# Optimization experiments

Measured on AMD Instinct MI355X. Metric: run time of the kernel, lower is better.

The kernel has to match this reference:

```python
import jax, jax.numpy as jnp
import numpy as np

B, N, E = 8, 10000, 320000
IN_DIM, E_H, E_OUT, OUT_DIM = 16, 32, 32, 32
D_EDGE_IN = IN_DIM * 2 + 2 + 1  # src feats + tgt feats + edge_attr_norm(2) + edge_weight(1)


def setup_inputs() -> dict:
    key = jax.random.key(0)
    ks = jax.random.split(key, 10)
    x = jax.random.normal(ks[0], (B, N, IN_DIM), dtype=jnp.float32)
    edge_index = jax.random.randint(ks[1], (2, E), 0, N)
    # col 0 = city_dist (kept >= 0.5 to avoid divide-by-tiny), col 1 = city_direc
    edge_attr = jax.random.uniform(ks[2], (E, 2), dtype=jnp.float32) + 0.5
    wind_mean = jax.random.normal(ks[3], (2,), dtype=jnp.float32)
    wind_std = jax.random.uniform(ks[4], (2,), dtype=jnp.float32) + 0.5
    def lin(k, fo, fi):
        return jax.random.normal(k, (fo, fi), dtype=jnp.float32) / np.sqrt(fi).astype(np.float32)
    W1 = lin(ks[5], E_H, D_EDGE_IN); b1 = jnp.zeros((E_H,), jnp.float32)
    W2 = lin(ks[6], E_OUT, E_H);     b2 = jnp.zeros((E_OUT,), jnp.float32)
    W3 = lin(ks[7], OUT_DIM, E_OUT); b3 = jnp.zeros((OUT_DIM,), jnp.float32)
    return dict(x=x, edge_attr=edge_attr, wind_mean=wind_mean, wind_std=wind_std,
                W1=W1, b1=b1, W2=W2, b2=b2, W3=W3, b3=b3, edge_index=edge_index)


def reference(x, edge_attr, wind_mean, wind_std, W1, b1, W2, b2, W3, b3, edge_index):
    edge_src, edge_tgt = edge_index[0], edge_index[1]
    node_src = x[:, edge_src]   # [B, E, D] gather
    node_tgt = x[:, edge_tgt]   # [B, E, D]
    # de-normalize wind (last two feature channels of source node)
    src_wind = node_src[:, :, -2:] * wind_std[None, None, :] + wind_mean[None, None, :]
    src_wind_speed = src_wind[:, :, 0]
    src_wind_direc = src_wind[:, :, 1]
    city_dist = edge_attr[:, 0][None, :]   # [1, E]
    city_direc = edge_attr[:, 1][None, :]
    theta = jnp.abs(city_direc - src_wind_direc)                       # [B, E]
    edge_weight = jax.nn.relu(3.0 * src_wind_speed * jnp.cos(theta * 360.0 / 16.0) / city_dist)
    # normalization of edge_attr uses torch's unbiased std (ddof=1)
    ea_norm = (edge_attr - edge_attr.mean(axis=0)) / edge_attr.std(axis=0, ddof=1)  # [E, 2]
    feat = jnp.concatenate([
        node_src, node_tgt,
        jnp.broadcast_to(ea_norm[None], (node_src.shape[0], E, 2)),
        edge_weight[:, :, None],
    ], axis=-1)                                                        # [B, E, D_EDGE_IN]
    h = jax.nn.sigmoid(jnp.einsum('bef,hf->beh', feat, W1) + b1)       # edge MLP
    h = jax.nn.sigmoid(jnp.einsum('beh,oh->beo', h, W2) + b2)          # [B, E, E_OUT]
    agg = jnp.zeros((x.shape[0], x.shape[1], h.shape[-1]), h.dtype).at[:, edge_tgt].add(h)
    out = jax.nn.sigmoid(jnp.einsum('bno,po->bnp', agg, W3) + b3)      # node MLP -> [B, N, OUT_DIM]
    return out
```

## Files before the change

kernel.cpp:

```cpp
#include <hip/hip_runtime.h>
#include <hip/hip_fp16.h>
#include <cmath>

constexpr int Bc = 8;
constexpr int Nn = 10000;
constexpr int Ec = 320000;
constexpr int IN = 16;
constexpr int EH = 32;
constexpr int EO = 32;
constexpr int OD = 32;

constexpr size_t U_CNT = 8;
constexpr size_t U_CUR = U_CNT + Nn;
constexpr size_t U_REC = 20016;
constexpr size_t U_PA  = U_REC + 4 * (size_t)Ec;
constexpr size_t U_PB  = U_PA + (size_t)Bc * Nn * 16;
constexpr size_t U_PW  = U_PB + (size_t)Bc * Nn * 16;

typedef short bf16x8 __attribute__((ext_vector_type(8)));
typedef float f32x4 __attribute__((ext_vector_type(4)));

__device__ __forceinline__ float sigmoid_f(float x) {
    return __builtin_amdgcn_rcpf(1.0f + __expf(-x));
}
__device__ __forceinline__ unsigned bf16r(float f) {
    unsigned u = __builtin_bit_cast(unsigned, f);
    return (u + 0x7FFFu + ((u >> 16) & 1u)) >> 16;
}
__device__ __forceinline__ unsigned bf16pk(float lo, float hi) {
    return bf16r(lo) | (bf16r(hi) << 16);
}

__global__ __launch_bounds__(256) void stats_hist_kernel(const float* __restrict__ ea,
                                                         const int* __restrict__ ei,
                                                         float* __restrict__ ws) {
    int* cnt = (int*)ws + U_CNT;
    float s0 = 0.f, s1 = 0.f, q0 = 0.f, q1 = 0.f;
    for (int i = blockIdx.x * blockDim.x + threadIdx.x; i < Ec; i += gridDim.x * blockDim.x) {
        float2 v = reinterpret_cast<const float2*>(ea)[i];
        s0 += v.x; s1 += v.y; q0 += v.x * v.x; q1 += v.y * v.y;
        atomicAdd(&cnt[ei[Ec + i]], 1);
    }
#pragma unroll
    for (int off = 32; off > 0; off >>= 1) {
        s0 += __shfl_down(s0, off);
        s1 += __shfl_down(s1, off);
        q0 += __shfl_down(q0, off);
        q1 += __shfl_down(q1, off);
    }
    if ((threadIdx.x & 63) == 0) {
        atomicAdd(&ws[0], s0);
        atomicAdd(&ws[1], s1);
        atomicAdd(&ws[2], q0);
        atomicAdd(&ws[3], q1);
    }
}

__global__ void scan_kernel(float* __restrict__ ws) {
    const int tid = threadIdx.x;
    const int lane = tid & 63;
    const int w = tid >> 6;
    if (tid == 0) {
        float s0 = ws[0], s1 = ws[1], q0 = ws[2], q1 = ws[3];
        float m0 = s0 / (float)Ec, m1 = s1 / (float)Ec;
        float v0 = (q0 - s0 * m0) / (float)(Ec - 1);
        float v1 = (q1 - s1 * m1) / (float)(Ec - 1);
        ws[4] = m0; ws[5] = m1;
        ws[6] = rsqrtf(v0); ws[7] = rsqrtf(v1);
    }
    int* cnt    = (int*)ws + U_CNT;
    int* cursor = (int*)ws + U_CUR;
    __shared__ int wtot[4];
    constexpr int CHUNK = 2560;
    const int lo = w * CHUNK;
    const int hi = min(Nn, lo + CHUNK);
    int sum = 0;
    for (int i = lo + lane; i < hi; i += 64) sum += cnt[i];
#pragma unroll
    for (int off = 32; off > 0; off >>= 1) sum += __shfl_down(sum, off);
    if (lane == 0) wtot[w] = sum;
    __syncthreads();
    int carry = 0;
    for (int k = 0; k < w; ++k) carry += wtot[k];
    for (int base = lo; base < hi; base += 64) {
        const int idx = base + lane;
        const int c = (idx < hi) ? cnt[idx] : 0;
        int v = c;
#pragma unroll
        for (int off = 1; off < 64; off <<= 1) {
            int u = __shfl_up(v, off);
            if (lane >= off) v += u;
        }
        if (idx < hi) cursor[idx] = carry + v - c;
        carry += __shfl(v, 63);
    }
}

__global__ __launch_bounds__(256) void record_kernel(const int* __restrict__ ei,
                                                     const float* __restrict__ ea,
                                                     float* __restrict__ ws) {
    int* cursor = (int*)ws + U_CUR;
    uint4* rec  = reinterpret_cast<uint4*>((unsigned*)ws + U_REC);
    const int e = blockIdx.x * 256 + threadIdx.x;
    const int src = ei[e];
    const int tgt = ei[Ec + e];
    const float2 v = reinterpret_cast<const float2*>(ea)[e];
    const int pos = atomicAdd(&cursor[tgt], 1);
    rec[pos] = make_uint4((unsigned)src, (unsigned)tgt,
                          __builtin_bit_cast(unsigned, v.x),
                          __builtin_bit_cast(unsigned, v.y));
}

__global__ __launch_bounds__(256) void precompute_kernel(
    const float* __restrict__ x, const float* __restrict__ wmean,
    const float* __restrict__ wstd, const float* __restrict__ W1,
    const float* __restrict__ b1, float* __restrict__ ws)
{
    const int idx = blockIdx.x * 256 + threadIdx.x;
    if (idx >= Bc * Nn) return;
    const float4* xr = reinterpret_cast<const float4*>(x + (size_t)idx * IN);
    float xv[16];
    float4 t;
    t = xr[0]; xv[0]  = t.x; xv[1]  = t.y; xv[2]  = t.z; xv[3]  = t.w;
    t = xr[1]; xv[4]  = t.x; xv[5]  = t.y; xv[6]  = t.z; xv[7]  = t.w;
    t = xr[2]; xv[8]  = t.x; xv[9]  = t.y; xv[10] = t.z; xv[11] = t.w;
    t = xr[3]; xv[12] = t.x; xv[13] = t.y; xv[14] = t.z; xv[15] = t.w;

    __half2* PA = reinterpret_cast<__half2*>((unsigned*)ws + U_PA) + (size_t)idx * 16;
    __half2* PB = reinterpret_cast<__half2*>((unsigned*)ws + U_PB) + (size_t)idx * 16;
#pragma unroll
    for (int p = 0; p < 16; ++p) {
        float a[2], bb[2];
#pragma unroll
        for (int j = 0; j < 2; ++j) {
            const int o = 2 * p + j;
            const float* wr = W1 + o * 35;
            float av = 0.f, bv = b1[o];
#pragma unroll
            for (int f = 0; f < 16; ++f) {
                av += xv[f] * wr[f];
                bv += xv[f] * wr[16 + f];
            }
            a[j] = av; bb[j] = bv;
        }
        PA[p] = __half2{__float2half(a[0]), __float2half(a[1])};
        PB[p] = __half2{__float2half(bb[0]), __float2half(bb[1])};
    }
    float2* PW = reinterpret_cast<float2*>((unsigned*)ws + U_PW);
    PW[idx] = make_float2(3.0f * (xv[14] * wstd[0] + wmean[0]),
                          xv[15] * wstd[1] + wmean[1]);
}

__global__ __launch_bounds__(256, 4) void edge_kernel(
    const float* __restrict__ W1, const float* __restrict__ W2,
    const float* __restrict__ b2, const float* __restrict__ ws,
    float* __restrict__ agg)
{
    __shared__ unsigned lds[4 * 2560];
    const int tid  = threadIdx.x;
    const int lane = tid & 63;
    const int wid  = tid >> 6;
    unsigned* wl = lds + wid * 2560;

    const int bid = blockIdx.x;
    const int b   = bid & 7;
    const int gid = (bid >> 3) * 256 + wid * 64 + lane;

    const unsigned* wsu = (const unsigned*)ws;
    const uint4 rec = reinterpret_cast<const uint4*>(wsu + U_REC)[gid];
    const int src = (int)rec.x;
    const int tgt = (int)rec.y;
    const float eax = __builtin_bit_cast(float, rec.z);
    const float eay = __builtin_bit_cast(float, rec.w);

    const float2 pw = reinterpret_cast<const float2*>(wsu + U_PW)[b * Nn + src];
    const float theta = fabsf(eay - pw.y);
    const float ewt = fmaxf(pw.x * __cosf(theta * 22.5f) * __builtin_amdgcn_rcpf(eax), 0.0f);
    const float f32v = (eax - ws[4]) * ws[6];
    const float f33v = (eay - ws[5]) * ws[7];

    const uint4* pa4 = reinterpret_cast<const uint4*>(wsu + U_PA + ((size_t)b * Nn + src) * 16);
    const uint4* pb4 = reinterpret_cast<const uint4*>(wsu + U_PB + ((size_t)b * Nn + tgt) * 16);

    unsigned hw[16];
#pragma unroll
    for (int q = 0; q < 4; ++q) {
        const uint4 ua = pa4[q];
        const uint4 ub = pb4[q];
        const unsigned au[4] = {ua.x, ua.y, ua.z, ua.w};
        const unsigned bu[4] = {ub.x, ub.y, ub.z, ub.w};
#pragma unroll
        for (int j = 0; j < 4; ++j) {
            const int p = 4 * q + j;
            const __half2 s = __hadd2(__builtin_bit_cast(__half2, au[j]),
                                      __builtin_bit_cast(__half2, bu[j]));
            const float2 f = __half22float2(s);
            const int o0 = 2 * p, o1 = 2 * p + 1;
            const float acc0 = f.x + f32v * W1[o0 * 35 + 32]
                                   + f33v * W1[o0 * 35 + 33]
                                   + ewt  * W1[o0 * 35 + 34];
            const float acc1 = f.y + f32v * W1[o1 * 35 + 32]
                                   + f33v * W1[o1 * 35 + 33]
                                   + ewt  * W1[o1 * 35 + 34];
            hw[p] = bf16pk(sigmoid_f(acc0), sigmoid_f(acc1));
        }
    }
    {
        uint4* hrow = reinterpret_cast<uint4*>(wl + lane * 20);
#pragma unroll
        for (int q = 0; q < 4; ++q)
            hrow[q] = make_uint4(hw[4*q], hw[4*q+1], hw[4*q+2], hw[4*q+3]);
    }

    const int tprev = __shfl_up(tgt, 1);
    const bool head = (lane == 0) || (tprev != tgt);
    const unsigned long long mask = __ballot(head);
    const unsigned long long mle = (~0ULL) >> (63 - lane);
    const int run = __popcll(mask & mle) - 1;
    const int nruns = __popcll(mask);
    wl[2432 + lane] = (unsigned)run;
    if (head) wl[2496 + run] = (unsigned)tgt;

    const int c16 = lane & 15;
    const int hq  = lane >> 4;

    bf16x8 bw[2];
#pragma unroll
    for (int t = 0; t < 2; ++t) {
        const float* wr = W2 + (c16 + 16 * t) * 32 + 8 * hq;
        const float4 w0 = *reinterpret_cast<const float4*>(wr);
        const float4 w1 = *reinterpret_cast<const float4*>(wr + 4);
        const uint4 pk = make_uint4(bf16pk(w0.x, w0.y), bf16pk(w0.z, w0.w),
                                    bf16pk(w1.x, w1.y), bf16pk(w1.z, w1.w));
        bw[t] = __builtin_bit_cast(bf16x8, pk);
    }

    f32x4 c[4][2];
#pragma unroll
    for (int m = 0; m < 4; ++m) {
        const uint4 av = *reinterpret_cast<const uint4*>(wl + (16 * m + c16) * 20 + 4 * hq);
        const bf16x8 afr = __builtin_bit_cast(bf16x8, av);
#pragma unroll
        for (int t = 0; t < 2; ++t) {
            f32x4 z = {0.f, 0.f, 0.f, 0.f};
            c[m][t] = __builtin_amdgcn_mfma_f32_16x16x32_bf16(afr, bw[t], z, 0, 0, 0);
        }
    }

    const float b2v[2] = { b2[c16], b2[c16 + 16] };
#pragma unroll
    for (int m = 0; m < 4; ++m) {
#pragma unroll
        for (int t = 0; t < 2; ++t) {
            const float v0 = sigmoid_f(c[m][t][0] + b2v[t]);
            const float v1 = sigmoid_f(c[m][t][1] + b2v[t]);
            const float v2 = sigmoid_f(c[m][t][2] + b2v[t]);
            const float v3 = sigmoid_f(c[m][t][3] + b2v[t]);
            const uint2 pk = make_uint2(bf16pk(v0, v1), bf16pk(v2, v3));
            *reinterpret_cast<uint2*>(wl + 1280 + (c16 + 16 * t) * 36 + 8 * m + 2 * hq) = pk;
        }
    }

    bf16x8 vb[2][2];
    unsigned rid[2][8];
#pragma unroll
    for (int kk = 0; kk < 2; ++kk) {
#pragma unroll
        for (int t = 0; t < 2; ++t) {
            const uint4 vv = *reinterpret_cast<const uint4*>(wl + 1280 + (c16 + 16 * t) * 36 + 16 * kk + 4 * hq);
            vb[kk][t] = __builtin_bit_cast(bf16x8, vv);
        }
        const uint4 r0 = *reinterpret_cast<const uint4*>(wl + 2432 + 32 * kk + 8 * hq);
        const uint4 r1 = *reinterpret_cast<const uint4*>(wl + 2432 + 32 * kk + 8 * hq + 4);
        rid[kk][0] = r0.x; rid[kk][1] = r0.y; rid[kk][2] = r0.z; rid[kk][3] = r0.w;
        rid[kk][4] = r1.x; rid[kk][5] = r1.y; rid[kk][6] = r1.z; rid[kk][7] = r1.w;
    }

    const int nm = (nruns + 15) >> 4;
    for (int mr = 0; mr < nm; ++mr) {
        const unsigned rowg = (unsigned)(16 * mr + c16);
        f32x4 d0 = {0.f, 0.f, 0.f, 0.f};
        f32x4 d1 = {0.f, 0.f, 0.f, 0.f};
#pragma unroll
        for (int kk = 0; kk < 2; ++kk) {
            unsigned iw[4];
#pragma unroll
            for (int w = 0; w < 4; ++w) {
                iw[w] = (rid[kk][2 * w]     == rowg ? 0x3f80u : 0u)
                      | (rid[kk][2 * w + 1] == rowg ? 0x3f800000u : 0u);
            }
            const bf16x8 ifr = __builtin_bit_cast(bf16x8, make_uint4(iw[0], iw[1], iw[2], iw[3]));
            d0 = __builtin_amdgcn_mfma_f32_16x16x32_bf16(ifr, vb[kk][0], d0, 0, 0, 0);
            d1 = __builtin_amdgcn_mfma_f32_16x16x32_bf16(ifr, vb[kk][1], d1, 0, 0, 0);
        }
#pragma unroll
        for (int r = 0; r < 4; ++r) {
            const int rn = 16 * mr + 4 * hq + r;
            const unsigned tr = wl[2496 + (rn & 63)];
            if (rn < nruns) {
                float* dst = agg + ((size_t)b * Nn + tr) * 32;
                atomicAdd(dst + c16,      d0[r]);
                atomicAdd(dst + c16 + 16, d1[r]);
            }
        }
    }
}

__global__ __launch_bounds__(256) void node_kernel(
    const float* __restrict__ W3, const float* __restrict__ b3,
    float* __restrict__ out)
{
    const int idx = blockIdx.x * 256 + threadIdx.x;
    if (idx >= Bc * Nn) return;
    float* row = out + (size_t)idx * OD;

    float a[EO];
#pragma unroll
    for (int i = 0; i < EO / 4; ++i) {
        float4 t = reinterpret_cast<float4*>(row)[i];
        a[4 * i] = t.x; a[4 * i + 1] = t.y; a[4 * i + 2] = t.z; a[4 * i + 3] = t.w;
    }
    float r[OD];
#pragma unroll
    for (int p = 0; p < OD; ++p) {
        const float* wr = W3 + p * EO;
        float s = b3[p];
#pragma unroll
        for (int o = 0; o < EO; ++o) s += a[o] * wr[o];
        r[p] = sigmoid_f(s);
    }
#pragma unroll
    for (int i = 0; i < OD / 4; ++i) {
        float4 t;
        t.x = r[4 * i + 0]; t.y = r[4 * i + 1];
        t.z = r[4 * i + 2]; t.w = r[4 * i + 3];
        reinterpret_cast<float4*>(row)[i] = t;
    }
}

extern "C" void kernel_launch(void* const* d_in, const int* in_sizes, int n_in,
                              void* d_out, int out_size, void* d_ws, size_t ws_size,
                              hipStream_t stream) {
    const float* x     = (const float*)d_in[0];
    const float* ea    = (const float*)d_in[1];
    const float* wmean = (const float*)d_in[2];
    const float* wstd  = (const float*)d_in[3];
    const float* W1    = (const float*)d_in[4];
    const float* b1    = (const float*)d_in[5];
    const float* W2    = (const float*)d_in[6];
    const float* b2    = (const float*)d_in[7];
    const float* W3    = (const float*)d_in[8];
    const float* b3    = (const float*)d_in[9];
    const int*   ei    = (const int*)d_in[10];
    float* out = (float*)d_out;
    float* ws  = (float*)d_ws;

    hipMemsetAsync(d_out, 0, (size_t)out_size * sizeof(float), stream);
    hipMemsetAsync(d_ws, 0, (U_CNT + Nn) * sizeof(float), stream);

    stats_hist_kernel<<<256, 256, 0, stream>>>(ea, ei, ws);
    scan_kernel<<<1, 256, 0, stream>>>(ws);
    record_kernel<<<Ec / 256, 256, 0, stream>>>(ei, ea, ws);
    precompute_kernel<<<(Bc * Nn + 255) / 256, 256, 0, stream>>>(x, wmean, wstd, W1, b1, ws);
    edge_kernel<<<(Ec / 256) * Bc, 256, 0, stream>>>(W1, W2, b2, ws, out);
    node_kernel<<<(Bc * Nn + 255) / 256, 256, 0, stream>>>(W3, b3, out);
}
```

Before: 234.0 us.

## Merge histogram, node precompute and output zeroing into one prep kernel; widen scan

Folds the edge-attribute stats/histogram, per-node W1 precompute and the output memset into a single launch whose blocks are partitioned by role. This cuts two launches and a memset and lets the independent stages run concurrently on the GPU. The single-block prefix scan moves from 256 threads looping over 64-wide chunks to 1024 threads, each doing a 10-element serial scan followed by wave and block scans, which shortens the serial scan latency. Mixing heterogeneous block roles in one grid can create some load imbalance.

```diff
diff --git a/kernel.cpp b/kernel.cpp
--- a/kernel.cpp
+++ b/kernel.cpp
@@ -17,6 +17,10 @@
 constexpr size_t U_PB  = U_PA + (size_t)Bc * Nn * 16;
 constexpr size_t U_PW  = U_PB + (size_t)Bc * Nn * 16;
 
+constexpr int HIST_BLOCKS = 256;
+constexpr int PRE_BLOCKS  = (Bc * Nn + 255) / 256;
+constexpr int ZERO_BLOCKS = 512;
+
 typedef short bf16x8 __attribute__((ext_vector_type(8)));
 typedef float f32x4 __attribute__((ext_vector_type(4)));
 
@@ -31,32 +35,84 @@
     return bf16r(lo) | (bf16r(hi) << 16);
 }
 
-__global__ __launch_bounds__(256) void stats_hist_kernel(const float* __restrict__ ea,
-                                                         const int* __restrict__ ei,
-                                                         float* __restrict__ ws) {
-    int* cnt = (int*)ws + U_CNT;
-    float s0 = 0.f, s1 = 0.f, q0 = 0.f, q1 = 0.f;
-    for (int i = blockIdx.x * blockDim.x + threadIdx.x; i < Ec; i += gridDim.x * blockDim.x) {
-        float2 v = reinterpret_cast<const float2*>(ea)[i];
-        s0 += v.x; s1 += v.y; q0 += v.x * v.x; q1 += v.y * v.y;
-        atomicAdd(&cnt[ei[Ec + i]], 1);
-    }
-#pragma unroll
-    for (int off = 32; off > 0; off >>= 1) {
-        s0 += __shfl_down(s0, off);
-        s1 += __shfl_down(s1, off);
-        q0 += __shfl_down(q0, off);
-        q1 += __shfl_down(q1, off);
-    }
-    if ((threadIdx.x & 63) == 0) {
-        atomicAdd(&ws[0], s0);
-        atomicAdd(&ws[1], s1);
-        atomicAdd(&ws[2], q0);
-        atomicAdd(&ws[3], q1);
-    }
-}
-
-__global__ void scan_kernel(float* __restrict__ ws) {
+__global__ __launch_bounds__(256) void prep_kernel(
+    const float* __restrict__ ea, const int* __restrict__ ei,
+    const float* __restrict__ x, const float* __restrict__ wmean,
+    const float* __restrict__ wstd, const float* __restrict__ W1,
+    const float* __restrict__ b1, float* __restrict__ ws,
+    float* __restrict__ out)
+{
+    const int blk = blockIdx.x;
+    const int tid = threadIdx.x;
+
+    if (blk < HIST_BLOCKS) {
+        int* cnt = (int*)ws + U_CNT;
+        const int lo = blk * (Ec / HIST_BLOCKS);
+        const int hi = lo + (Ec / HIST_BLOCKS);
+        float s0 = 0.f, s1 = 0.f, q0 = 0.f, q1 = 0.f;
+        for (int i = lo + tid; i < hi; i += 256) {
+            float2 v = reinterpret_cast<const float2*>(ea)[i];
+            s0 += v.x; s1 += v.y; q0 += v.x * v.x; q1 += v.y * v.y;
+            atomicAdd(&cnt[ei[Ec + i]], 1);
+        }
+#pragma unroll
+        for (int off = 32; off > 0; off >>= 1) {
+            s0 += __shfl_down(s0, off);
+            s1 += __shfl_down(s1, off);
+            q0 += __shfl_down(q0, off);
+            q1 += __shfl_down(q1, off);
+        }
+        if ((tid & 63) == 0) {
+            atomicAdd(&ws[0], s0);
+            atomicAdd(&ws[1], s1);
+            atomicAdd(&ws[2], q0);
+            atomicAdd(&ws[3], q1);
+        }
+    } else if (blk < HIST_BLOCKS + PRE_BLOCKS) {
+        const int idx = (blk - HIST_BLOCKS) * 256 + tid;
+        if (idx >= Bc * Nn) return;
+        const float4* xr = reinterpret_cast<const float4*>(x + (size_t)idx * IN);
+        float xv[16];
+        float4 t;
+        t = xr[0]; xv[0]  = t.x; xv[1]  = t.y; xv[2]  = t.z; xv[3]  = t.w;
+        t = xr[1]; xv[4]  = t.x; xv[5]  = t.y; xv[6]  = t.z; xv[7]  = t.w;
+        t = xr[2]; xv[8]  = t.x; xv[9]  = t.y; xv[10] = t.z; xv[11] = t.w;
+        t = xr[3]; xv[12] = t.x; xv[13] = t.y; xv[14] = t.z; xv[15] = t.w;
+
+        __half2* PA = reinterpret_cast<__half2*>((unsigned*)ws + U_PA) + (size_t)idx * 16;
+        __half2* PB = reinterpret_cast<__half2*>((unsigned*)ws + U_PB) + (size_t)idx * 16;
+#pragma unroll
+        for (int p = 0; p < 16; ++p) {
+            float a[2], bb[2];
+#pragma unroll
+            for (int j = 0; j < 2; ++j) {
+                const int o = 2 * p + j;
+                const float* wr = W1 + o * 35;
+                float av = 0.f, bv = b1[o];
+#pragma unroll
+                for (int f = 0; f < 16; ++f) {
+                    av += xv[f] * wr[f];
+                    bv += xv[f] * wr[16 + f];
+                }
+                a[j] = av; bb[j] = bv;
+            }
+            PA[p] = __half2{__float2half(a[0]), __float2half(a[1])};
+            PB[p] = __half2{__float2half(bb[0]), __float2half(bb[1])};
+        }
+        float2* PW = reinterpret_cast<float2*>((unsigned*)ws + U_PW);
+        PW[idx] = make_float2(3.0f * (xv[14] * wstd[0] + wmean[0]),
+                              xv[15] * wstd[1] + wmean[1]);
+    } else {
+        float4* o4 = reinterpret_cast<float4*>(out);
+        constexpr int TOT4 = Bc * Nn * 32 / 4;
+        const float4 z = make_float4(0.f, 0.f, 0.f, 0.f);
+        for (int i = (blk - HIST_BLOCKS - PRE_BLOCKS) * 256 + tid; i < TOT4;
+             i += ZERO_BLOCKS * 256)
+            o4[i] = z;
+    }
+}
+
+__global__ __launch_bounds__(1024) void scan_kernel(float* __restrict__ ws) {
     const int tid = threadIdx.x;
     const int lane = tid & 63;
     const int w = tid >> 6;
@@ -70,29 +126,44 @@
     }
     int* cnt    = (int*)ws + U_CNT;
     int* cursor = (int*)ws + U_CUR;
-    __shared__ int wtot[4];
-    constexpr int CHUNK = 2560;
-    const int lo = w * CHUNK;
-    const int hi = min(Nn, lo + CHUNK);
+
+    constexpr int PER = 10;
+    const int lo = tid * PER;
+    int local[PER];
     int sum = 0;
-    for (int i = lo + lane; i < hi; i += 64) sum += cnt[i];
-#pragma unroll
-    for (int off = 32; off > 0; off >>= 1) sum += __shfl_down(sum, off);
-    if (lane == 0) wtot[w] = sum;
+#pragma unroll
+    for (int k = 0; k < PER; ++k) {
+        const int i = lo + k;
+        const int c = (i < Nn) ? cnt[i] : 0;
+        local[k] = sum;
+        sum += c;
+    }
+    int v = sum;
+#pragma unroll
+    for (int off = 1; off < 64; off <<= 1) {
+        int u = __shfl_up(v, off);
+        if (lane >= off) v += u;
+    }
+    __shared__ int wt[16];
+    __shared__ int woff[16];
+    if (lane == 63) wt[w] = v;
     __syncthreads();
-    int carry = 0;
-    for (int k = 0; k < w; ++k) carry += wtot[k];
-    for (int base = lo; base < hi; base += 64) {
-        const int idx = base + lane;
-        const int c = (idx < hi) ? cnt[idx] : 0;
-        int v = c;
-#pragma unroll
-        for (int off = 1; off < 64; off <<= 1) {
-            int u = __shfl_up(v, off);
-            if (lane >= off) v += u;
-        }
-        if (idx < hi) cursor[idx] = carry + v - c;
-        carry += __shfl(v, 63);
+    if (w == 0) {
+        int t = (lane < 16) ? wt[lane] : 0;
+        int tv = t;
+#pragma unroll
+        for (int off = 1; off < 16; off <<= 1) {
+            int u = __shfl_up(tv, off);
+            if (lane >= off) tv += u;
+        }
+        if (lane < 16) woff[lane] = tv - t;
+    }
+    __syncthreads();
+    const int base = woff[w] + (v - sum);
+#pragma unroll
+    for (int k = 0; k < PER; ++k) {
+        const int i = lo + k;
+        if (i < Nn) cursor[i] = base + local[k];
     }
 }
 
@@ -109,46 +180,6 @@
     rec[pos] = make_uint4((unsigned)src, (unsigned)tgt,
                           __builtin_bit_cast(unsigned, v.x),
                           __builtin_bit_cast(unsigned, v.y));
-}
-
-__global__ __launch_bounds__(256) void precompute_kernel(
-    const float* __restrict__ x, const float* __restrict__ wmean,
-    const float* __restrict__ wstd, const float* __restrict__ W1,
-    const float* __restrict__ b1, float* __restrict__ ws)
-{
-    const int idx = blockIdx.x * 256 + threadIdx.x;
-    if (idx >= Bc * Nn) return;
-    const float4* xr = reinterpret_cast<const float4*>(x + (size_t)idx * IN);
-    float xv[16];
-    float4 t;
-    t = xr[0]; xv[0]  = t.x; xv[1]  = t.y; xv[2]  = t.z; xv[3]  = t.w;
-    t = xr[1]; xv[4]  = t.x; xv[5]  = t.y; xv[6]  = t.z; xv[7]  = t.w;
-    t = xr[2]; xv[8]  = t.x; xv[9]  = t.y; xv[10] = t.z; xv[11] = t.w;
-    t = xr[3]; xv[12] = t.x; xv[13] = t.y; xv[14] = t.z; xv[15] = t.w;
-
-    __half2* PA = reinterpret_cast<__half2*>((unsigned*)ws + U_PA) + (size_t)idx * 16;
-    __half2* PB = reinterpret_cast<__half2*>((unsigned*)ws + U_PB) + (size_t)idx * 16;
-#pragma unroll
-    for (int p = 0; p < 16; ++p) {
-        float a[2], bb[2];
-#pragma unroll
-        for (int j = 0; j < 2; ++j) {
-            const int o = 2 * p + j;
-            const float* wr = W1 + o * 35;
-            float av = 0.f, bv = b1[o];
-#pragma unroll
-            for (int f = 0; f < 16; ++f) {
-                av += xv[f] * wr[f];
-                bv += xv[f] * wr[16 + f];
-            }
-            a[j] = av; bb[j] = bv;
-        }
-        PA[p] = __half2{__float2half(a[0]), __float2half(a[1])};
-        PB[p] = __half2{__float2half(bb[0]), __float2half(bb[1])};
-    }
-    float2* PW = reinterpret_cast<float2*>((unsigned*)ws + U_PW);
-    PW[idx] = make_float2(3.0f * (xv[14] * wstd[0] + wmean[0]),
-                          xv[15] * wstd[1] + wmean[1]);
 }
 
 __global__ __launch_bounds__(256, 4) void edge_kernel(
@@ -355,13 +386,12 @@
     float* out = (float*)d_out;
     float* ws  = (float*)d_ws;
 
-    hipMemsetAsync(d_out, 0, (size_t)out_size * sizeof(float), stream);
     hipMemsetAsync(d_ws, 0, (U_CNT + Nn) * sizeof(float), stream);
 
-    stats_hist_kernel<<<256, 256, 0, stream>>>(ea, ei, ws);
-    scan_kernel<<<1, 256, 0, stream>>>(ws);
+    prep_kernel<<<HIST_BLOCKS + PRE_BLOCKS + ZERO_BLOCKS, 256, 0, stream>>>(
+        ea, ei, x, wmean, wstd, W1, b1, ws, out);
+    scan_kernel<<<1, 1024, 0, stream>>>(ws);
     record_kernel<<<Ec / 256, 256, 0, stream>>>(ei, ea, ws);
-    precompute_kernel<<<(Bc * Nn + 255) / 256, 256, 0, stream>>>(x, wmean, wstd, W1, b1, ws);
     edge_kernel<<<(Ec / 256) * Bc, 256, 0, stream>>>(W1, W2, b2, ws, out);
     node_kernel<<<(Bc * Nn + 255) / 256, 256, 0, stream>>>(W3, b3, out);
 }
```

Result: faster. 204.7 us (-12.5%).
